# Optimization experiments

Measured on AMD Instinct MI355X. Metric: run time of the kernel, lower is better.

## Reference

```python
import jax, jax.numpy as jnp
import numpy as np

# Model hyperparameters (match init_kwargs)
N_HEADS = 16
N_KV_HEADS = 4
HEAD_DIM = 128
ROPE_THETA = 10000.0
WINDOW = 1024  # sliding window (left), right window = 0
SOFTCAP = 50.0
B, T, C = 2, 2048, 2048
G = N_HEADS // N_KV_HEADS


def _sine_table(features, length, max_timescale):
    # min_timescale = 1.0 in the original
    fraction = jnp.arange(0, features, 2, dtype=jnp.float32) / features
    inv_timescale = 1.0 / (max_timescale ** fraction)
    sinusoid = jnp.einsum('i,j->ij', jnp.arange(length), inv_timescale,
                          precision=jax.lax.Precision.HIGHEST)
    sinusoid = jnp.concatenate([sinusoid, sinusoid], axis=-1)  # [T, H]
    return jnp.sin(sinusoid), jnp.cos(sinusoid)


def _rotate_half(x):
    x1, x2 = jnp.split(x, 2, axis=-1)
    return jnp.concatenate([-x2, x1], axis=-1)


def setup_inputs() -> dict:
    key = jax.random.key(0)
    kx, kq, kk, kv, ko = jax.random.split(key, 5)
    x = jax.random.normal(kx, (B, T, C), dtype=jnp.float32)
    init = lambda k, shape: 0.02 * jax.random.normal(k, shape, dtype=jnp.float32)
    q_kernel = init(kq, (C, N_HEADS * HEAD_DIM))
    k_kernel = init(kk, (C, N_KV_HEADS * HEAD_DIM))
    v_kernel = init(kv, (C, N_KV_HEADS * HEAD_DIM))
    out_kernel = init(ko, (N_HEADS * HEAD_DIM, C))
    return {"x": x, "q_kernel": q_kernel, "k_kernel": k_kernel,
            "v_kernel": v_kernel, "out_kernel": out_kernel}


def _attention(x, q_kernel, k_kernel, v_kernel, out_kernel):
    Bs, Ts, Cs = x.shape
    K, H, Gn = N_KV_HEADS, HEAD_DIM, G
    q = jnp.dot(x, q_kernel).reshape(Bs, Ts, K, Gn, H)
    k = jnp.dot(x, k_kernel).reshape(Bs, Ts, K, H)
    v = jnp.dot(x, v_kernel).reshape(Bs, Ts, K, H)

    # RoPE: cos/sin broadcast along the T axis (axis 1), over heads.
    sin, cos = _sine_table(H, Ts, ROPE_THETA)
    qcos = cos[None, :, None, None, :]
    qsin = sin[None, :, None, None, :]
    kcos = cos[None, :, None, :]
    ksin = sin[None, :, None, :]
    q = (q * qcos + _rotate_half(q) * qsin).astype(q.dtype)
    k = (k * kcos + _rotate_half(k) * ksin).astype(k.dtype)

    # Causal + sliding-window mask: key <= query <= key + WINDOW
    pos = jnp.arange(Ts)
    mask = (pos[:, None] >= pos[None, :]) & (pos[:, None] <= pos[None, :] + WINDOW)
    mask = mask[None, None, :, :]  # [1,1,T,S]
    neg = jnp.asarray(-0.7 * jnp.finfo(jnp.float32).max, dtype=jnp.float32)

    scale = jnp.asarray(H ** (-0.5), dtype=q.dtype)
    encoded = []
    for i in range(Gn):  # fixed, small group loop (matches GQA structure)
        qi = q[:, :, :, i] * scale                              # [B,T,K,H]
        logits = jnp.einsum('BTKH,BSKH->BKTS', qi, k)
        logits = jnp.tanh(logits / SOFTCAP) * SOFTCAP           # softcap
        logits = jnp.where(mask, logits, neg)
        probs = jax.nn.softmax(logits.astype(jnp.float32), axis=-1).astype(logits.dtype)
        encoded.append(jnp.einsum('BKTS,BSKH->BTKH', probs, v))
    encoded = jnp.stack(encoded, axis=3)                        # [B,T,K,G,H]
    encoded = encoded.reshape(Bs, Ts, N_HEADS * H)
    return jnp.dot(encoded, out_kernel)


def reference(x, q_kernel, k_kernel, v_kernel, out_kernel):
    return _attention(x, q_kernel, k_kernel, v_kernel, out_kernel)
```

## Files before the change

kernel.cpp:

```cpp
#include <hip/hip_runtime.h>
#include <hip/hip_bf16.h>
#include <math.h>

#define BB 2
#define TT 2048
#define CC 2048
#define NH 16
#define NKV 4
#define HD 128
#define BT (BB*TT)
#define WINDOW 1024
#define SQKV 3072

typedef unsigned short u16;
typedef unsigned int u32;
typedef __attribute__((ext_vector_type(8))) short short8;
typedef __attribute__((ext_vector_type(8))) unsigned short ushort8;
typedef __attribute__((ext_vector_type(4))) unsigned short ushort4v;
typedef __attribute__((ext_vector_type(2))) unsigned int uint2v;
typedef __attribute__((ext_vector_type(4))) float floatx4;
typedef __attribute__((ext_vector_type(16))) float floatx16;

typedef const __attribute__((address_space(1))) u32* gas_ptr;
typedef __attribute__((address_space(3))) u32* las_ptr;

static __device__ __forceinline__ u16 f2bf(float f) {
    unsigned u = __builtin_bit_cast(unsigned, f);
    return (u16)((u + 0x7fffu + ((u >> 16) & 1u)) >> 16);
}
static __device__ __forceinline__ float bf2f(u16 v) {
    unsigned u = ((unsigned)v) << 16;
    return __builtin_bit_cast(float, u);
}

static __device__ __forceinline__ u32 cvt_pk_bf16(float lo, float hi) {
    u32 r;
    asm("v_cvt_pk_bf16_f32 %0, %1, %2" : "=v"(r) : "v"(lo), "v"(hi));
    return r;
}

static __device__ __forceinline__ float softcap_exp(float s) {
    float t = s * 0.02f;
    t = fmaxf(-1.0f, fminf(1.0f, t));
    float t2 = t * t;
    float e = t * fmaf(t2, fmaf(t2, 9.617967f, -24.044917f), 72.134752f);
    return __builtin_amdgcn_exp2f(e);
}

__global__ void cast_bf16_kernel(const float* __restrict__ in, u16* __restrict__ out, int n4) {
    int i = blockIdx.x * blockDim.x + threadIdx.x;
    if (i >= n4) return;
    floatx4 v = *(const floatx4*)(in + (size_t)i * 4);
    ushort4v o;
    o[0] = f2bf(v[0]); o[1] = f2bf(v[1]); o[2] = f2bf(v[2]); o[3] = f2bf(v[3]);
    *(ushort4v*)(out + (size_t)i * 4) = o;
}

__global__ void transpose_cast_f32_kernel(const float* __restrict__ in, u16* __restrict__ out,
                                          int R, int Cc) {
    __shared__ u16 tile[32][33];
    int c0 = blockIdx.x * 32, r0 = blockIdx.y * 32;
    int tx = threadIdx.x, ty = threadIdx.y;
    #pragma unroll
    for (int i = 0; i < 4; i++) {
        int r = r0 + ty + i * 8;
        tile[ty + i * 8][tx] = f2bf(in[(size_t)r * Cc + c0 + tx]);
    }
    __syncthreads();
    #pragma unroll
    for (int i = 0; i < 4; i++) {
        int c = c0 + ty + i * 8;
        out[(size_t)c * R + r0 + tx] = tile[tx][ty + i * 8];
    }
}

__global__ void transpose_bf16_kernel(const u16* __restrict__ in, u16* __restrict__ out,
                                      int R, int Cc, int inStride, int colOff,
                                      size_t inBatchStride, size_t outBatchStride) {
    __shared__ u16 tile[32][33];
    int b = blockIdx.z;
    const u16* inb = in + (size_t)b * inBatchStride;
    u16* outb = out + (size_t)b * outBatchStride;
    int c0 = blockIdx.y * 32, r0 = blockIdx.x * 32;
    int tx = threadIdx.x, ty = threadIdx.y;
    #pragma unroll
    for (int i = 0; i < 4; i++) {
        int r = r0 + ty + i * 8;
        tile[ty + i * 8][tx] = inb[(size_t)r * inStride + colOff + c0 + tx];
    }
    __syncthreads();
    #pragma unroll
    for (int i = 0; i < 4; i++) {
        int c = c0 + ty + i * 8;
        outb[(size_t)c * R + r0 + tx] = tile[tx][ty + i * 8];
    }
}

__global__ void rope_kernel(u16* __restrict__ buf, int H, int rowStride, float scale) {
    int idx = blockIdx.x;
    int bt = idx / H, h = idx - bt * H;
    int t = bt % TT;
    int d = threadIdx.x;
    u16* p = buf + (size_t)bt * rowStride + h * HD;
    float x  = bf2f(p[d]);
    float xp = bf2f(p[d ^ 64]);
    int j = d & 63;
    float inv = exp2f(-0.20762050593046f * (float)j);
    float ang = (float)t * inv;
    float s, c;
    sincosf(ang, &s, &c);
    float rot = (d < 64) ? -xp : xp;
    float o = (x * c + rot * s) * scale;
    __syncthreads();
    p[d] = f2bf(o);
}

template <bool OUT_F32>
__global__ __launch_bounds__(256) void gemm128_kernel(const u16* __restrict__ A,
                                                      const u16* __restrict__ Bt,
                                                      void* __restrict__ Cout,
                                                      int M, int N, int K) {
    __shared__ alignas(16) u16 As[128 * 32];
    __shared__ alignas(16) u16 Bs[128 * 32];
    int tid = threadIdx.x;
    int w = tid >> 6, lane = tid & 63, quad = lane >> 4, ln = lane & 15;
    int m0 = blockIdx.y * 128;
    int n0 = blockIdx.x * 128;
    int wm = (w >> 1) * 64;
    int wn = (w & 1) * 64;

    int o0 = (w * 2) * 1024 + lane * 16;
    int row0 = o0 >> 6, kc0 = (o0 & 63) >> 4;
    int o1 = o0 + 1024;
    int row1 = o1 >> 6, kc1 = (o1 & 63) >> 4;
    const u16* gA0 = A  + (size_t)(m0 + row0) * K + kc0 * 8;
    const u16* gA1 = A  + (size_t)(m0 + row1) * K + kc1 * 8;
    const u16* gB0 = Bt + (size_t)(n0 + row0) * K + kc0 * 8;
    const u16* gB1 = Bt + (size_t)(n0 + row1) * K + kc1 * 8;
    u16* lA0 = As + (w * 2) * 512;
    u16* lA1 = As + (w * 2 + 1) * 512;
    u16* lB0 = Bs + (w * 2) * 512;
    u16* lB1 = Bs + (w * 2 + 1) * 512;

    floatx4 acc[4][4] = {};

    for (int k0 = 0; k0 < K; k0 += 32) {
        __syncthreads();
        __builtin_amdgcn_global_load_lds((gas_ptr)(gA0 + k0), (las_ptr)lA0, 16, 0, 0);
        __builtin_amdgcn_global_load_lds((gas_ptr)(gA1 + k0), (las_ptr)lA1, 16, 0, 0);
        __builtin_amdgcn_global_load_lds((gas_ptr)(gB0 + k0), (las_ptr)lB0, 16, 0, 0);
        __builtin_amdgcn_global_load_lds((gas_ptr)(gB1 + k0), (las_ptr)lB1, 16, 0, 0);
        __syncthreads();

        short8 af[4], bf[4];
        #pragma unroll
        for (int mt = 0; mt < 4; mt++)
            af[mt] = *(const short8*)(As + (wm + mt * 16 + ln) * 32 + quad * 8);
        #pragma unroll
        for (int nt = 0; nt < 4; nt++)
            bf[nt] = *(const short8*)(Bs + (wn + nt * 16 + ln) * 32 + quad * 8);
        #pragma unroll
        for (int mt = 0; mt < 4; mt++)
            #pragma unroll
            for (int nt = 0; nt < 4; nt++)
                acc[mt][nt] = __builtin_amdgcn_mfma_f32_16x16x32_bf16(af[mt], bf[nt], acc[mt][nt], 0, 0, 0);
    }

    #pragma unroll
    for (int mt = 0; mt < 4; mt++)
      #pragma unroll
      for (int nt = 0; nt < 4; nt++)
        #pragma unroll
        for (int r = 0; r < 4; r++) {
            size_t row = m0 + wm + mt * 16 + quad * 4 + r;
            size_t col = n0 + wn + nt * 16 + ln;
            float v = acc[mt][nt][r];
            if (OUT_F32) ((float*)Cout)[row * N + col] = v;
            else         ((u16*)Cout)[row * N + col] = f2bf(v);
        }
}

__global__ __launch_bounds__(256, 2) void attn_kernel(const u16* __restrict__ QKV,
                                                      const u16* __restrict__ Vt,
                                                      u16* __restrict__ Enc) {
    __shared__ alignas(16) u16 pool[2 * 8192];

    int tid = threadIdx.x;
    int w = tid >> 6, lane = tid & 63, hi = lane >> 5, ln = lane & 31;
    int hi8 = hi * 8;

    int qb = (15 - (int)blockIdx.x) * 128;
    int bh = blockIdx.y;
    int b = bh >> 4, h = bh & 15, kh = h >> 2;
    int qw = qb + w * 32;

    short8 qf[8];
    {
        const u16* qptr = QKV + (size_t)(b * TT + qw + ln) * SQKV + h * HD + hi8;
        #pragma unroll
        for (int ks = 0; ks < 8; ks++) qf[ks] = *(const short8*)(qptr + ks * 16);
    }

    int sig = (ln & 3) + (((ln >> 3) & 1) << 2) + (((ln >> 2) & 1) << 3) + ((ln >> 4) << 4);
    bool isK = (w < 2);
    const u16* dsrc[4];
    int ldst[4];
    #pragma unroll
    for (int i = 0; i < 4; i++) {
        if (isK) {
            int ks = w * 4 + i;
            dsrc[i] = QKV + (size_t)(b * TT + sig) * SQKV + 2048 + kh * HD + ks * 16 + hi8;
            ldst[i] = ks * 512;
        } else {
            int g = (w - 2) * 4 + i;
            dsrc[i] = Vt + (size_t)((b * NKV + kh) * HD + (g >> 1) * 32 + ln) * TT + (g & 1) * 16 + hi8;
            ldst[i] = 4096 + g * 512;
        }
    }
    size_t addmul = isK ? (size_t)SQKV : (size_t)1;

    floatx16 O0 = {}, O1 = {}, O2 = {}, O3 = {};
    float lacc = 0.0f;

    int S_LO = qb - WINDOW; if (S_LO < 0) S_LO = 0;
    int nt = (qb + 128 - S_LO) >> 5;

    auto issue = [&](int t) {
        int s0 = S_LO + t * 32;
        u16* base = pool + (t & 1) * 8192;
        size_t add = (size_t)s0 * addmul;
        #pragma unroll
        for (int i = 0; i < 4; i++)
            __builtin_amdgcn_global_load_lds((gas_ptr)(dsrc[i] + add), (las_ptr)(base + ldst[i]), 16, 0, 0);
    };

    issue(0);
    for (int t = 0; t < nt; ++t) {
        __builtin_amdgcn_sched_barrier(0);
        __builtin_amdgcn_s_barrier();
        __builtin_amdgcn_sched_barrier(0);
        if (t + 1 < nt) {
            issue(t + 1);
            __builtin_amdgcn_sched_barrier(0);
            __builtin_amdgcn_s_waitcnt(0x0F74);
        } else {
            __builtin_amdgcn_s_waitcnt(0x0F70);
        }
        __builtin_amdgcn_sched_barrier(0);
        __builtin_amdgcn_s_barrier();
        __builtin_amdgcn_sched_barrier(0);

        int s0 = S_LO + t * 32;
        if (s0 > qw + 31 || s0 + 31 < qw - WINDOW) continue;

        const u16* Kb = pool + (t & 1) * 8192;
        const u16* Vb = Kb + 4096;

        floatx16 S = {};
        #pragma unroll
        for (int ks = 0; ks < 8; ks++) {
            short8 kf = *(const short8*)(Kb + ks * 512 + lane * 8);
            S = __builtin_amdgcn_mfma_f32_32x32x16_bf16(kf, qf[ks], S, 0, 0, 0);
        }

        bool full = (s0 + 31 <= qw) && (s0 >= qw + 31 - WINDOW);
        if (full) {
            #pragma unroll
            for (int r = 0; r < 16; r++) S[r] = softcap_exp(S[r]);
        } else {
            int tq = qw + ln;
            #pragma unroll
            for (int r = 0; r < 16; r++) {
                int s = s0 + (r & 3) + (((r >> 2) & 1) << 2) + hi8 + ((r >> 3) << 4);
                bool good = (s <= tq) && (s >= tq - WINDOW);
                S[r] = good ? softcap_exp(S[r]) : 0.0f;
            }
        }

        lacc += ((((S[0] + S[1]) + (S[2] + S[3])) + ((S[4] + S[5]) + (S[6] + S[7])))
               + (((S[8] + S[9]) + (S[10] + S[11])) + ((S[12] + S[13]) + (S[14] + S[15]))));

        u32 w0a = cvt_pk_bf16(S[0],  S[1]),  w0b = cvt_pk_bf16(S[2],  S[3]);
        u32 w0c = cvt_pk_bf16(S[4],  S[5]),  w0d = cvt_pk_bf16(S[6],  S[7]);
        u32 w1a = cvt_pk_bf16(S[8],  S[9]),  w1b = cvt_pk_bf16(S[10], S[11]);
        u32 w1c = cvt_pk_bf16(S[12], S[13]), w1d = cvt_pk_bf16(S[14], S[15]);
        typedef __attribute__((ext_vector_type(4))) unsigned int u32x4t;
        u32x4t pw0 = { w0a, w0b, w0c, w0d };
        u32x4t pw1 = { w1a, w1b, w1c, w1d };
        short8 pf0 = __builtin_bit_cast(short8, pw0);
        short8 pf1 = __builtin_bit_cast(short8, pw1);

        #pragma unroll
        for (int dt = 0; dt < 4; dt++) {
            short8 vf0 = *(const short8*)(Vb + (dt * 2 + 0) * 512 + lane * 8);
            short8 vf1 = *(const short8*)(Vb + (dt * 2 + 1) * 512 + lane * 8);
            floatx16* Od = (dt == 0) ? &O0 : (dt == 1) ? &O1 : (dt == 2) ? &O2 : &O3;
            *Od = __builtin_amdgcn_mfma_f32_32x32x16_bf16(vf0, pf0, *Od, 0, 0, 0);
            *Od = __builtin_amdgcn_mfma_f32_32x32x16_bf16(vf1, pf1, *Od, 0, 0, 0);
        }
    }

    __syncthreads();

    lacc += __shfl_xor(lacc, 32);
    float inv = __builtin_amdgcn_rcpf(lacc);
    u16* ep = pool + w * 1024;
    const floatx16* Os[4] = { &O0, &O1, &O2, &O3 };
    #pragma unroll
    for (int dt = 0; dt < 4; dt++) {
        #pragma unroll
        for (int g = 0; g < 4; g++) {
            float a0 = (*Os[dt])[g * 4 + 0] * inv, a1 = (*Os[dt])[g * 4 + 1] * inv;
            float a2 = (*Os[dt])[g * 4 + 2] * inv, a3 = (*Os[dt])[g * 4 + 3] * inv;
            uint2v pk;
            pk[0] = cvt_pk_bf16(a0, a1);
            pk[1] = cvt_pk_bf16(a2, a3);
            *(uint2v*)(ep + ln * 32 + g * 8 + hi * 4) = pk;
        }
        ushort8 r0 = *(const ushort8*)(ep + ln * 32 + hi * 16);
        ushort8 r1 = *(const ushort8*)(ep + ln * 32 + hi * 16 + 8);
        u16* dst = Enc + (size_t)(b * TT + qw + ln) * (NH * HD) + h * HD + dt * 32 + hi * 16;
        *(ushort8*)dst = r0;
        *(ushort8*)(dst + 8) = r1;
    }
}

extern "C" void kernel_launch(void* const* d_in, const int* in_sizes, int n_in,
                              void* d_out, int out_size, void* d_ws, size_t ws_size,
                              hipStream_t stream) {
    const float* x  = (const float*)d_in[0];
    const float* wq = (const float*)d_in[1];
    const float* wk = (const float*)d_in[2];
    const float* wv = (const float*)d_in[3];
    const float* wo = (const float*)d_in[4];
    float* out = (float*)d_out;

    char* ws = (char*)d_ws;
    size_t off = 0;
    auto alloc = [&](size_t bytes) -> void* {
        void* p = ws + off;
        off += (bytes + 255) & ~(size_t)255;
        return p;
    };
    u16* xb    = (u16*)alloc((size_t)BT * CC * 2);
    u16* wqkvT = (u16*)alloc((size_t)SQKV * CC * 2);
    u16* woT   = (u16*)alloc((size_t)CC * CC * 2);
    u16* QKVb  = (u16*)alloc((size_t)BT * SQKV * 2);
    u16* VtT   = (u16*)alloc((size_t)BT * NKV * HD * 2);
    u16* Enc   = (u16*)alloc((size_t)BT * NH * HD * 2);

    cast_bf16_kernel<<<(BT * CC / 4 + 255) / 256, 256, 0, stream>>>(x, xb, BT * CC / 4);
    dim3 tb(32, 8);
    transpose_cast_f32_kernel<<<dim3(CC / 32, CC / 32), tb, 0, stream>>>(wq, wqkvT, CC, CC);
    transpose_cast_f32_kernel<<<dim3(NKV * HD / 32, CC / 32), tb, 0, stream>>>(wk, wqkvT + (size_t)2048 * CC, CC, NKV * HD);
    transpose_cast_f32_kernel<<<dim3(NKV * HD / 32, CC / 32), tb, 0, stream>>>(wv, wqkvT + (size_t)2560 * CC, CC, NKV * HD);
    transpose_cast_f32_kernel<<<dim3(CC / 32, CC / 32), tb, 0, stream>>>(wo, woT, CC, CC);

    gemm128_kernel<false><<<dim3(SQKV / 128, BT / 128), 256, 0, stream>>>(xb, wqkvT, QKVb, BT, SQKV, CC);

    rope_kernel<<<BT * NH, HD, 0, stream>>>(QKVb, NH, SQKV, 0.08838834764831845f);
    rope_kernel<<<BT * NKV, HD, 0, stream>>>(QKVb + 2048, NKV, SQKV, 1.0f);

    transpose_bf16_kernel<<<dim3(TT / 32, NKV * HD / 32, BB), tb, 0, stream>>>(
        QKVb, VtT, TT, NKV * HD, SQKV, 2560,
        (size_t)TT * SQKV, (size_t)NKV * HD * TT);

    attn_kernel<<<dim3(16, 32), 256, 0, stream>>>(QKVb, VtT, Enc);

    gemm128_kernel<true><<<dim3(CC / 128, BT / 128), 256, 0, stream>>>(Enc, woT, out, BT, CC, CC);
}
```

Measured before the change: 329.6 us.

## Rewrite GEMM as 512-thread double-buffered pipeline with K=64 stages

Replaces the 256-thread single-buffered GEMM with a 512-thread (8-wave) version that double-buffers 64-wide K tiles in LDS, issuing the next stage's direct global-to-LDS loads while computing the current one. LDS is laid out in pre-swizzled 16x32 fragment blocks, so each lane reads its MFMA operand contiguously, and s_setprio is raised around the MFMA section. This targets load latency and barrier stalls in the QKV and output projections. In exchange it uses 64 KB of LDS per block, which limits occupancy, and relies on hand-written waitcnt encodings for correctness.

```diff
diff --git a/kernel.cpp b/kernel.cpp
--- a/kernel.cpp
+++ b/kernel.cpp
@@ -116,65 +116,98 @@
 }
 
 template <bool OUT_F32>
-__global__ __launch_bounds__(256) void gemm128_kernel(const u16* __restrict__ A,
-                                                      const u16* __restrict__ Bt,
-                                                      void* __restrict__ Cout,
-                                                      int M, int N, int K) {
-    __shared__ alignas(16) u16 As[128 * 32];
-    __shared__ alignas(16) u16 Bs[128 * 32];
+__global__ __launch_bounds__(512, 4) void gemm128x8_kernel(const u16* __restrict__ A,
+                                                           const u16* __restrict__ Bt,
+                                                           void* __restrict__ Cout,
+                                                           int M, int N, int K) {
+    __shared__ alignas(16) u16 lds[2 * 16384];
     int tid = threadIdx.x;
     int w = tid >> 6, lane = tid & 63, quad = lane >> 4, ln = lane & 15;
+    int wm = w >> 2, wn = w & 3;
     int m0 = blockIdx.y * 128;
     int n0 = blockIdx.x * 128;
-    int wm = (w >> 1) * 64;
-    int wn = (w & 1) * 64;
-
-    int o0 = (w * 2) * 1024 + lane * 16;
-    int row0 = o0 >> 6, kc0 = (o0 & 63) >> 4;
-    int o1 = o0 + 1024;
-    int row1 = o1 >> 6, kc1 = (o1 & 63) >> 4;
-    const u16* gA0 = A  + (size_t)(m0 + row0) * K + kc0 * 8;
-    const u16* gA1 = A  + (size_t)(m0 + row1) * K + kc1 * 8;
-    const u16* gB0 = Bt + (size_t)(n0 + row0) * K + kc0 * 8;
-    const u16* gB1 = Bt + (size_t)(n0 + row1) * K + kc1 * 8;
-    u16* lA0 = As + (w * 2) * 512;
-    u16* lA1 = As + (w * 2 + 1) * 512;
-    u16* lB0 = Bs + (w * 2) * 512;
-    u16* lB1 = Bs + (w * 2 + 1) * 512;
-
-    floatx4 acc[4][4] = {};
-
-    for (int k0 = 0; k0 < K; k0 += 32) {
-        __syncthreads();
-        __builtin_amdgcn_global_load_lds((gas_ptr)(gA0 + k0), (las_ptr)lA0, 16, 0, 0);
-        __builtin_amdgcn_global_load_lds((gas_ptr)(gA1 + k0), (las_ptr)lA1, 16, 0, 0);
-        __builtin_amdgcn_global_load_lds((gas_ptr)(gB0 + k0), (las_ptr)lB0, 16, 0, 0);
-        __builtin_amdgcn_global_load_lds((gas_ptr)(gB1 + k0), (las_ptr)lB1, 16, 0, 0);
-        __syncthreads();
-
-        short8 af[4], bf[4];
-        #pragma unroll
-        for (int mt = 0; mt < 4; mt++)
-            af[mt] = *(const short8*)(As + (wm + mt * 16 + ln) * 32 + quad * 8);
-        #pragma unroll
-        for (int nt = 0; nt < 4; nt++)
-            bf[nt] = *(const short8*)(Bs + (wn + nt * 16 + ln) * 32 + quad * 8);
-        #pragma unroll
-        for (int mt = 0; mt < 4; mt++)
+
+    const u16* gsrc[4];
+    #pragma unroll
+    for (int j = 0; j < 4; j++) {
+        int g = j * 8 + w;
+        int gl = g & 15;
+        int mf = gl >> 1, ks = gl & 1;
+        const u16* base = (g < 16) ? (A + (size_t)m0 * K) : (Bt + (size_t)n0 * K);
+        gsrc[j] = base + (size_t)(mf * 16 + ln) * K + ks * 32 + quad * 8;
+    }
+    int ldst = w * 512 + lane * 8;
+
+    floatx4 acc[4][2] = {};
+    int nk = K >> 6;
+
+    auto stage = [&](int t) {
+        u16* dst = lds + (t & 1) * 16384;
+        int k0 = t * 64;
+        #pragma unroll
+        for (int j = 0; j < 4; j++)
+            __builtin_amdgcn_global_load_lds((gas_ptr)(gsrc[j] + k0),
+                                             (las_ptr)(dst + j * 4096 + ldst), 16, 0, 0);
+    };
+
+    stage(0);
+    stage(1);
+    __builtin_amdgcn_s_waitcnt(0x0F74);
+    __builtin_amdgcn_sched_barrier(0);
+    __builtin_amdgcn_s_barrier();
+    __builtin_amdgcn_sched_barrier(0);
+
+    for (int t = 0; t < nk; ++t) {
+        const u16* buf = lds + (t & 1) * 16384;
+
+        short8 bfr[2][2];
+        #pragma unroll
+        for (int n = 0; n < 2; n++)
             #pragma unroll
-            for (int nt = 0; nt < 4; nt++)
-                acc[mt][nt] = __builtin_amdgcn_mfma_f32_16x16x32_bf16(af[mt], bf[nt], acc[mt][nt], 0, 0, 0);
-    }
-
-    #pragma unroll
-    for (int mt = 0; mt < 4; mt++)
+            for (int ks = 0; ks < 2; ks++)
+                bfr[n][ks] = *(const short8*)(buf + 8192 + ((wn * 2 + n) * 2 + ks) * 512 + lane * 8);
+
+        __builtin_amdgcn_s_setprio(1);
+        #pragma unroll
+        for (int m = 0; m < 4; m++) {
+            short8 af0 = *(const short8*)(buf + ((wm * 4 + m) * 2 + 0) * 512 + lane * 8);
+            short8 af1 = *(const short8*)(buf + ((wm * 4 + m) * 2 + 1) * 512 + lane * 8);
+            #pragma unroll
+            for (int n = 0; n < 2; n++) {
+                acc[m][n] = __builtin_amdgcn_mfma_f32_16x16x32_bf16(af0, bfr[n][0], acc[m][n], 0, 0, 0);
+                acc[m][n] = __builtin_amdgcn_mfma_f32_16x16x32_bf16(af1, bfr[n][1], acc[m][n], 0, 0, 0);
+            }
+        }
+        __builtin_amdgcn_s_setprio(0);
+
+        __builtin_amdgcn_sched_barrier(0);
+        __builtin_amdgcn_s_barrier();
+        __builtin_amdgcn_sched_barrier(0);
+
+        if (t + 2 < nk) {
+            stage(t + 2);
+            __builtin_amdgcn_sched_barrier(0);
+            __builtin_amdgcn_s_waitcnt(0x0F74);
+            __builtin_amdgcn_sched_barrier(0);
+            __builtin_amdgcn_s_barrier();
+            __builtin_amdgcn_sched_barrier(0);
+        } else if (t + 1 < nk) {
+            __builtin_amdgcn_s_waitcnt(0x0F70);
+            __builtin_amdgcn_sched_barrier(0);
+            __builtin_amdgcn_s_barrier();
+            __builtin_amdgcn_sched_barrier(0);
+        }
+    }
+
+    #pragma unroll
+    for (int m = 0; m < 4; m++)
       #pragma unroll
-      for (int nt = 0; nt < 4; nt++)
+      for (int n = 0; n < 2; n++)
         #pragma unroll
         for (int r = 0; r < 4; r++) {
-            size_t row = m0 + wm + mt * 16 + quad * 4 + r;
-            size_t col = n0 + wn + nt * 16 + ln;
-            float v = acc[mt][nt][r];
+            size_t row = m0 + wm * 64 + m * 16 + quad * 4 + r;
+            size_t col = n0 + wn * 32 + n * 16 + ln;
+            float v = acc[m][n][r];
             if (OUT_F32) ((float*)Cout)[row * N + col] = v;
             else         ((u16*)Cout)[row * N + col] = f2bf(v);
         }
@@ -356,7 +389,7 @@
     transpose_cast_f32_kernel<<<dim3(NKV * HD / 32, CC / 32), tb, 0, stream>>>(wv, wqkvT + (size_t)2560 * CC, CC, NKV * HD);
     transpose_cast_f32_kernel<<<dim3(CC / 32, CC / 32), tb, 0, stream>>>(wo, woT, CC, CC);
 
-    gemm128_kernel<false><<<dim3(SQKV / 128, BT / 128), 256, 0, stream>>>(xb, wqkvT, QKVb, BT, SQKV, CC);
+    gemm128x8_kernel<false><<<dim3(SQKV / 128, BT / 128), 512, 0, stream>>>(xb, wqkvT, QKVb, BT, SQKV, CC);
 
     rope_kernel<<<BT * NH, HD, 0, stream>>>(QKVb, NH, SQKV, 0.08838834764831845f);
     rope_kernel<<<BT * NKV, HD, 0, stream>>>(QKVb + 2048, NKV, SQKV, 1.0f);
@@ -367,5 +400,5 @@
 
     attn_kernel<<<dim3(16, 32), 256, 0, stream>>>(QKVb, VtT, Enc);
 
-    gemm128_kernel<true><<<dim3(CC / 128, BT / 128), 256, 0, stream>>>(Enc, woT, out, BT, CC, CC);
-}
+    gemm128x8_kernel<true><<<dim3(CC / 128, BT / 128), 512, 0, stream>>>(Enc, woT, out, BT, CC, CC);
+}
```

Measured after the change: 363.2 us. 10.2% more time.

## Replace GEMM with 128x256-tile, 8-wave, multi-stage pipelined LDS kernel

Applied to the files above, without the earlier changes.

Replaces the 128x128 single-buffered GEMM with a 128x256 tile kernel using 512 threads. It issues async global-to-LDS loads three stages ahead across a double buffer, with explicit waitcnt and barrier scheduling plus setprio around the MFMA blocks. It also swizzles block IDs to group neighbouring tiles for L2 reuse. The aim is to hide global load latency behind compute and lower the load-to-MFMA ratio for both projection GEMMs. This adds fragile hand-tuned wait counts and fewer, larger blocks, so fewer workgroups can share the GPU.

```diff
diff --git a/kernel.cpp b/kernel.cpp
--- a/kernel.cpp
+++ b/kernel.cpp
@@ -116,65 +116,94 @@
 }
 
 template <bool OUT_F32>
-__global__ __launch_bounds__(256) void gemm128_kernel(const u16* __restrict__ A,
-                                                      const u16* __restrict__ Bt,
-                                                      void* __restrict__ Cout,
-                                                      int M, int N, int K) {
-    __shared__ alignas(16) u16 As[128 * 32];
-    __shared__ alignas(16) u16 Bs[128 * 32];
+__global__ __launch_bounds__(512, 2) void gemm256_kernel(const u16* __restrict__ A,
+                                                         const u16* __restrict__ Bt,
+                                                         void* __restrict__ Cout,
+                                                         int M, int N, int K) {
+    __shared__ alignas(16) u16 lds[2 * 24576];
     int tid = threadIdx.x;
     int w = tid >> 6, lane = tid & 63, quad = lane >> 4, ln = lane & 15;
-    int m0 = blockIdx.y * 128;
-    int n0 = blockIdx.x * 128;
-    int wm = (w >> 1) * 64;
-    int wn = (w & 1) * 64;
-
-    int o0 = (w * 2) * 1024 + lane * 16;
-    int row0 = o0 >> 6, kc0 = (o0 & 63) >> 4;
-    int o1 = o0 + 1024;
-    int row1 = o1 >> 6, kc1 = (o1 & 63) >> 4;
-    const u16* gA0 = A  + (size_t)(m0 + row0) * K + kc0 * 8;
-    const u16* gA1 = A  + (size_t)(m0 + row1) * K + kc1 * 8;
-    const u16* gB0 = Bt + (size_t)(n0 + row0) * K + kc0 * 8;
-    const u16* gB1 = Bt + (size_t)(n0 + row1) * K + kc1 * 8;
-    u16* lA0 = As + (w * 2) * 512;
-    u16* lA1 = As + (w * 2 + 1) * 512;
-    u16* lB0 = Bs + (w * 2) * 512;
-    u16* lB1 = Bs + (w * 2 + 1) * 512;
+    int wm = w >> 2, wn = w & 3;
+
+    int gx = gridDim.x;
+    int bid = blockIdx.y * gx + blockIdx.x;
+    int cpx = (gx * gridDim.y) >> 3;
+    int swz = (bid & 7) * cpx + (bid >> 3);
+    int m0 = (swz / gx) * 128;
+    int n0 = (swz - (swz / gx) * gx) * 256;
+
+    const u16* pA  = A  + (size_t)(m0 + w * 16 + ln) * K + quad * 8;
+    const u16* pB0 = Bt + (size_t)(n0 + w * 16 + ln) * K + quad * 8;
+    const u16* pB1 = Bt + (size_t)(n0 + (8 + w) * 16 + ln) * K + quad * 8;
+    int dA  = w * 1024 + lane * 8;
+    int dB0 = 8192 + w * 1024 + lane * 8;
+    int dB1 = 8192 + (8 + w) * 1024 + lane * 8;
+
+    int aoff = wm * 4096 + lane * 8;
+    int boff = 8192 + wn * 4096 + lane * 8;
 
     floatx4 acc[4][4] = {};
-
-    for (int k0 = 0; k0 < K; k0 += 32) {
-        __syncthreads();
-        __builtin_amdgcn_global_load_lds((gas_ptr)(gA0 + k0), (las_ptr)lA0, 16, 0, 0);
-        __builtin_amdgcn_global_load_lds((gas_ptr)(gA1 + k0), (las_ptr)lA1, 16, 0, 0);
-        __builtin_amdgcn_global_load_lds((gas_ptr)(gB0 + k0), (las_ptr)lB0, 16, 0, 0);
-        __builtin_amdgcn_global_load_lds((gas_ptr)(gB1 + k0), (las_ptr)lB1, 16, 0, 0);
-        __syncthreads();
-
+    const int nk = K >> 6;
+
+    auto stage = [&](int Y) {
+        int ty = Y >> 1, ks = Y & 1;
+        int koff = ty * 64 + ks * 32;
+        int bufo = (ty & 1) * 24576 + ks * 512;
+        __builtin_amdgcn_global_load_lds((gas_ptr)(pA  + koff), (las_ptr)(lds + bufo + dA),  16, 0, 0);
+        __builtin_amdgcn_global_load_lds((gas_ptr)(pB0 + koff), (las_ptr)(lds + bufo + dB0), 16, 0, 0);
+        __builtin_amdgcn_global_load_lds((gas_ptr)(pB1 + koff), (las_ptr)(lds + bufo + dB1), 16, 0, 0);
+    };
+
+    auto phase = [&](int t, int ks, int wait, bool doStage, bool doBar) {
+        const u16* buf = lds + (t & 1) * 24576 + ks * 512;
         short8 af[4], bf[4];
         #pragma unroll
-        for (int mt = 0; mt < 4; mt++)
-            af[mt] = *(const short8*)(As + (wm + mt * 16 + ln) * 32 + quad * 8);
-        #pragma unroll
-        for (int nt = 0; nt < 4; nt++)
-            bf[nt] = *(const short8*)(Bs + (wn + nt * 16 + ln) * 32 + quad * 8);
-        #pragma unroll
-        for (int mt = 0; mt < 4; mt++)
+        for (int m = 0; m < 4; m++) af[m] = *(const short8*)(buf + aoff + m * 1024);
+        #pragma unroll
+        for (int n = 0; n < 4; n++) bf[n] = *(const short8*)(buf + boff + n * 1024);
+        if (doStage) stage(2 * t + ks + 3);
+        __builtin_amdgcn_s_waitcnt(0xC07F);
+        __builtin_amdgcn_sched_barrier(0);
+        __builtin_amdgcn_s_setprio(1);
+        #pragma unroll
+        for (int m = 0; m < 4; m++)
             #pragma unroll
-            for (int nt = 0; nt < 4; nt++)
-                acc[mt][nt] = __builtin_amdgcn_mfma_f32_16x16x32_bf16(af[mt], bf[nt], acc[mt][nt], 0, 0, 0);
-    }
-
-    #pragma unroll
-    for (int mt = 0; mt < 4; mt++)
+            for (int n = 0; n < 4; n++)
+                acc[m][n] = __builtin_amdgcn_mfma_f32_16x16x32_bf16(af[m], bf[n], acc[m][n], 0, 0, 0);
+        __builtin_amdgcn_s_setprio(0);
+        __builtin_amdgcn_sched_barrier(0);
+        if (wait == 6)      __builtin_amdgcn_s_waitcnt(0x0F76);
+        else if (wait == 3) __builtin_amdgcn_s_waitcnt(0x0F73);
+        else if (wait == 0) __builtin_amdgcn_s_waitcnt(0x0F70);
+        __builtin_amdgcn_sched_barrier(0);
+        if (doBar) __builtin_amdgcn_s_barrier();
+        __builtin_amdgcn_sched_barrier(0);
+    };
+
+    stage(0); stage(1); stage(2);
+    __builtin_amdgcn_s_waitcnt(0x0F76);
+    __builtin_amdgcn_sched_barrier(0);
+    __builtin_amdgcn_s_barrier();
+    __builtin_amdgcn_sched_barrier(0);
+
+    for (int t = 0; t < nk - 2; ++t) {
+        phase(t, 0, 6, true, true);
+        phase(t, 1, 6, true, true);
+    }
+    phase(nk - 2, 0, 6, true,  true);
+    phase(nk - 2, 1, 3, false, true);
+    phase(nk - 1, 0, 0, false, true);
+    phase(nk - 1, 1, -1, false, false);
+
+    #pragma unroll
+    for (int m = 0; m < 4; m++)
       #pragma unroll
-      for (int nt = 0; nt < 4; nt++)
+      for (int n = 0; n < 4; n++)
         #pragma unroll
         for (int r = 0; r < 4; r++) {
-            size_t row = m0 + wm + mt * 16 + quad * 4 + r;
-            size_t col = n0 + wn + nt * 16 + ln;
-            float v = acc[mt][nt][r];
+            size_t row = m0 + wm * 64 + m * 16 + quad * 4 + r;
+            size_t col = n0 + wn * 64 + n * 16 + ln;
+            float v = acc[m][n][r];
             if (OUT_F32) ((float*)Cout)[row * N + col] = v;
             else         ((u16*)Cout)[row * N + col] = f2bf(v);
         }
@@ -356,7 +385,7 @@
     transpose_cast_f32_kernel<<<dim3(NKV * HD / 32, CC / 32), tb, 0, stream>>>(wv, wqkvT + (size_t)2560 * CC, CC, NKV * HD);
     transpose_cast_f32_kernel<<<dim3(CC / 32, CC / 32), tb, 0, stream>>>(wo, woT, CC, CC);
 
-    gemm128_kernel<false><<<dim3(SQKV / 128, BT / 128), 256, 0, stream>>>(xb, wqkvT, QKVb, BT, SQKV, CC);
+    gemm256_kernel<false><<<dim3(SQKV / 256, BT / 128), 512, 0, stream>>>(xb, wqkvT, QKVb, BT, SQKV, CC);
 
     rope_kernel<<<BT * NH, HD, 0, stream>>>(QKVb, NH, SQKV, 0.08838834764831845f);
     rope_kernel<<<BT * NKV, HD, 0, stream>>>(QKVb + 2048, NKV, SQKV, 1.0f);
@@ -367,5 +396,5 @@
 
     attn_kernel<<<dim3(16, 32), 256, 0, stream>>>(QKVb, VtT, Enc);
 
-    gemm128_kernel<true><<<dim3(CC / 128, BT / 128), 256, 0, stream>>>(Enc, woT, out, BT, CC, CC);
-}
+    gemm256_kernel<true><<<dim3(CC / 256, BT / 128), 512, 0, stream>>>(Enc, woT, out, BT, CC, CC);
+}
```

New measurement: 353.5 us. 1.07x slower.

## Use 256x256-tile pipelined GEMM with block swizzle for QKV projection

Applied to the files above, without the earlier changes.

Adds a new GEMM kernel with 256x256 output tiles, 8 waves, double-buffered direct global-to-LDS loads interleaved with MFMA phases, and an XCD-aware block swizzle. It is used for the fused QKV projection in place of the 128x128 GEMM. The larger tiles raise data reuse per LDS load and the staged prefetch overlaps memory with compute. The grid shrinks to 12x16=192 blocks, fewer than the CU count, and occupancy drops to one block per CU.

```diff
diff --git a/kernel.cpp b/kernel.cpp
--- a/kernel.cpp
+++ b/kernel.cpp
@@ -180,6 +180,103 @@
         }
 }
 
+template <bool OUT_F32>
+__global__ __launch_bounds__(512, 1) void gemm256sq_kernel(const u16* __restrict__ A,
+                                                           const u16* __restrict__ Bt,
+                                                           void* __restrict__ Cout,
+                                                           int M, int N, int K) {
+    __shared__ alignas(16) u16 lds[2 * 32768];
+    int tid = threadIdx.x;
+    int w = tid >> 6, lane = tid & 63, quad = lane >> 4, ln = lane & 15;
+    int wm = w >> 2, wn = w & 3;
+
+    int gx = gridDim.x;
+    int bid = blockIdx.y * gx + blockIdx.x;
+    int cpx = (gx * gridDim.y) >> 3;
+    int swz = (bid & 7) * cpx + (bid >> 3);
+    int m0 = (swz / gx) * 256;
+    int n0 = (swz - (swz / gx) * gx) * 256;
+
+    const u16* srcA0 = A  + (size_t)(m0 + w * 16 + ln) * K + quad * 8;
+    const u16* srcA1 = A  + (size_t)(m0 + 128 + w * 16 + ln) * K + quad * 8;
+    const u16* srcB0 = Bt + (size_t)(n0 + w * 16 + ln) * K + quad * 8;
+    const u16* srcB1 = Bt + (size_t)(n0 + 128 + w * 16 + ln) * K + quad * 8;
+    int dst0 = w * 512 + lane * 8;
+
+    floatx4 acc[8][4] = {};
+    short8 bfr[4];
+    const int nk = K >> 6;
+
+    auto stage = [&](int t, int ht) {
+        int ks = ht >> 1;
+        int ko = t * 64 + ks * 32;
+        const u16* s0 = (ht & 1) ? srcB0 : srcA0;
+        const u16* s1 = (ht & 1) ? srcB1 : srcA1;
+        u16* d = lds + (t & 1) * 32768 + ht * 8192 + dst0;
+        __builtin_amdgcn_global_load_lds((gas_ptr)(s0 + ko), (las_ptr)(d), 16, 0, 0);
+        __builtin_amdgcn_global_load_lds((gas_ptr)(s1 + ko), (las_ptr)(d + 4096), 16, 0, 0);
+    };
+
+    auto phase = [&](int t, int mh, int ks, int stht, int wait, bool bar) {
+        const u16* buf = lds + (t & 1) * 32768;
+        const u16* Ar = buf + ks * 16384 + (wm * 8 + mh * 4) * 512 + lane * 8;
+        const u16* Br = buf + 8192 + ks * 16384 + (wn * 4) * 512 + lane * 8;
+        short8 af[4];
+        #pragma unroll
+        for (int m = 0; m < 4; m++) af[m] = *(const short8*)(Ar + m * 512);
+        if (mh == 0) {
+            #pragma unroll
+            for (int n = 0; n < 4; n++) bfr[n] = *(const short8*)(Br + n * 512);
+        }
+        if (stht >= 0) stage(t + 1, stht);
+        __builtin_amdgcn_s_waitcnt(0xC07F);
+        __builtin_amdgcn_sched_barrier(0);
+        __builtin_amdgcn_s_setprio(1);
+        #pragma unroll
+        for (int m = 0; m < 4; m++)
+            #pragma unroll
+            for (int n = 0; n < 4; n++)
+                acc[mh * 4 + m][n] = __builtin_amdgcn_mfma_f32_16x16x32_bf16(af[m], bfr[n], acc[mh * 4 + m][n], 0, 0, 0);
+        __builtin_amdgcn_s_setprio(0);
+        if (wait == 4)      { __builtin_amdgcn_s_waitcnt(0x0F74); __builtin_amdgcn_sched_barrier(0); }
+        else if (wait == 0) { __builtin_amdgcn_s_waitcnt(0x0F70); __builtin_amdgcn_sched_barrier(0); }
+        if (bar) { __builtin_amdgcn_s_barrier(); __builtin_amdgcn_sched_barrier(0); }
+    };
+
+    stage(0, 0); stage(0, 1); stage(0, 2); stage(0, 3);
+    __builtin_amdgcn_s_waitcnt(0x0F74);
+    __builtin_amdgcn_sched_barrier(0);
+    __builtin_amdgcn_s_barrier();
+    __builtin_amdgcn_sched_barrier(0);
+
+    for (int t = 0; t < nk - 1; ++t) {
+        phase(t, 0, 0, 0, -1, false);
+        phase(t, 1, 0, 1,  4, true);
+        phase(t, 0, 1, 2, -1, false);
+        phase(t, 1, 1, 3,  4, true);
+    }
+    {
+        int t = nk - 1;
+        phase(t, 0, 0, -1, -1, false);
+        phase(t, 1, 0, -1,  0, true);
+        phase(t, 0, 1, -1, -1, false);
+        phase(t, 1, 1, -1, -1, false);
+    }
+
+    #pragma unroll
+    for (int mf = 0; mf < 8; mf++)
+      #pragma unroll
+      for (int n = 0; n < 4; n++)
+        #pragma unroll
+        for (int r = 0; r < 4; r++) {
+            size_t row = m0 + wm * 128 + mf * 16 + quad * 4 + r;
+            size_t col = n0 + wn * 64 + n * 16 + ln;
+            float v = acc[mf][n][r];
+            if (OUT_F32) ((float*)Cout)[row * N + col] = v;
+            else         ((u16*)Cout)[row * N + col] = f2bf(v);
+        }
+}
+
 __global__ __launch_bounds__(256, 2) void attn_kernel(const u16* __restrict__ QKV,
                                                       const u16* __restrict__ Vt,
                                                       u16* __restrict__ Enc) {
@@ -356,7 +453,7 @@
     transpose_cast_f32_kernel<<<dim3(NKV * HD / 32, CC / 32), tb, 0, stream>>>(wv, wqkvT + (size_t)2560 * CC, CC, NKV * HD);
     transpose_cast_f32_kernel<<<dim3(CC / 32, CC / 32), tb, 0, stream>>>(wo, woT, CC, CC);
 
-    gemm128_kernel<false><<<dim3(SQKV / 128, BT / 128), 256, 0, stream>>>(xb, wqkvT, QKVb, BT, SQKV, CC);
+    gemm256sq_kernel<false><<<dim3(SQKV / 256, BT / 256), 512, 0, stream>>>(xb, wqkvT, QKVb, BT, SQKV, CC);
 
     rope_kernel<<<BT * NH, HD, 0, stream>>>(QKVb, NH, SQKV, 0.08838834764831845f);
     rope_kernel<<<BT * NKV, HD, 0, stream>>>(QKVb + 2048, NKV, SQKV, 1.0f);
```

New measurement: 330.1 us. About the same (+0.2%).
